# Kernel optimization log

Measured on AMD Instinct MI355X. Metric: run time of the kernel, lower is better.

Reference implementation:

```python
import jax, jax.numpy as jnp
import numpy as np

S, L, E = 64, 256, 768          # sentences, tokens per sentence, BERT hidden
N, P = 4096, 32768              # events, event pairs
C, H, D = 256, 4, 64            # CGE channels, heads, head dim (C = H*D = n_last)
M = 8                           # max event span length
MLP_H = 1024
ITERS = 3                       # max_iteration + 1
RATE = 0.5
BETA_INTRA, BETA_INTER = 0.5, 0.5


def setup_inputs():
    key = jax.random.key(0)
    ks = jax.random.split(key, 16)
    nrm = lambda k, shape, sc: jax.random.normal(k, shape, dtype=jnp.float32) * sc
    event_start = jax.random.randint(ks[2], (N,), 0, L - M)
    span = jax.random.randint(ks[3], (N,), 1, M + 1)
    return {
        "sent_emb": nrm(ks[0], (S, L, E), 1.0),
        "proj_in_W": nrm(ks[7], (E, C), E ** -0.5),
        "proj_in_b": jnp.zeros((C,), jnp.float32),
        "proj_W": nrm(ks[8], (C, C), C ** -0.5),
        "proj_b": jnp.zeros((C,), jnp.float32),
        "att_src_intra": nrm(ks[9], (H, D), D ** -0.5),
        "att_dst_intra": nrm(ks[10], (H, D), D ** -0.5),
        "att_src_inter": nrm(ks[11], (H, D), D ** -0.5),
        "att_dst_inter": nrm(ks[12], (H, D), D ** -0.5),
        "mlp_W1": nrm(ks[13], (C + 2 * E, MLP_H), (C + 2 * E) ** -0.5),
        "mlp_b1": jnp.zeros((MLP_H,), jnp.float32),
        "mlp_W2": nrm(ks[14], (MLP_H, 3), MLP_H ** -0.5),
        "mlp_b2": jnp.zeros((3,), jnp.float32),
        "event_sent": jax.random.randint(ks[1], (N,), 0, S),
        "event_start": event_start,
        "event_end": event_start + span,
        "pair_idx": jax.random.randint(ks[4], (P, 2), 0, N),
        "rel_type": jax.random.randint(ks[5], (P,), 0, 2),
        "target": jax.random.randint(ks[6], (P,), 0, 3),
    }


def _attend(h, src, dst, emask, att_src, att_dst):
    # h: [N,H,D]. Masked graph attention, softmax over incoming edges per dst.
    a = jax.nn.leaky_relu((h[src] * att_src).sum(-1) + (h[dst] * att_dst).sum(-1), 0.2)  # [En,H]
    a = jnp.where(emask[:, None], a, -1e9)
    amax = jnp.maximum(jax.ops.segment_max(a, dst, num_segments=N), -1e9)  # [N,H]
    ex = jnp.exp(a - amax[dst]) * emask[:, None].astype(a.dtype)
    denom = jax.ops.segment_sum(ex, dst, num_segments=N)
    alpha = ex / (denom[dst] + 1e-9)
    out = jax.ops.segment_sum(alpha[:, :, None] * h[src], dst, num_segments=N)  # [N,H,D]
    return out.reshape(N, H * D)


def _forward(sent_emb, proj_in_W, proj_in_b, proj_W, proj_b,
             att_src_intra, att_dst_intra, att_src_inter, att_dst_inter,
             mlp_W1, mlp_b1, mlp_W2, mlp_b2,
             event_sent, event_start, event_end, pair_idx, rel_type, target):
    # extract_event: mean of sentence token embeddings over each event span
    pos = event_start[:, None] + jnp.arange(M)                      # [N,M]
    vmask = (pos < event_end[:, None]).astype(sent_emb.dtype)       # [N,M]
    tok = sent_emb[event_sent[:, None], jnp.clip(pos, 0, L - 1)]    # [N,M,E]
    e_emb = (tok * vmask[..., None]).sum(1) / (event_end - event_start).astype(sent_emb.dtype)[:, None]

    p0, p1 = pair_idx[:, 0], pair_idx[:, 1]
    pair_emb = jnp.concatenate([e_emb[p0], e_emb[p1]], axis=-1)     # [P,2E]
    x = e_emb @ proj_in_W + proj_in_b                               # [N,C]

    self_idx = jnp.arange(N)
    ones_n = jnp.ones((N,), bool)
    src_all = jnp.concatenate([p0, p1])
    dst_all = jnp.concatenate([p1, p0])
    intra2 = jnp.concatenate([rel_type == 0, rel_type == 0])

    loss = jnp.float32(0.0)
    pred = None
    for it in range(ITERS):
        diff = x[p0] - x[p1]                                        # [P,C]
        pre = jnp.concatenate([pair_emb, diff], axis=-1)            # [P,2E+C]
        pred = jax.nn.relu(pre @ mlp_W1 + mlp_b1) @ mlp_W2 + mlp_b2  # [P,3]
        logp = jax.nn.log_softmax(pred, axis=-1)
        loss = loss + (1.0 / (it + 1)) * (-jnp.take_along_axis(logp, target[:, None], axis=1).mean())

        # data-dependent edge construction (masked, fixed-size edge lists)
        psoft = jax.nn.softmax(pred, axis=-1)
        conf = psoft.max(1) > RATE
        parg = psoft.argmax(1)
        m_all = jnp.concatenate([conf & (parg == 1), conf & (parg == 2)])

        h = (x @ proj_W + proj_b).reshape(N, H, D)
        # intra edges + always-on self loops
        src_i = jnp.concatenate([src_all, self_idx])
        dst_i = jnp.concatenate([dst_all, self_idx])
        m_i = jnp.concatenate([m_all & intra2, ones_n])
        out_intra = _attend(h, src_i, dst_i, m_i, att_src_intra, att_dst_intra)
        out_inter = _attend(h, src_all, dst_all, m_all & (~intra2), att_src_inter, att_dst_inter)
        x = BETA_INTRA * out_intra + BETA_INTER * out_inter
    return loss, pred


def reference(sent_emb, proj_in_W, proj_in_b, proj_W, proj_b,
              att_src_intra, att_dst_intra, att_src_inter, att_dst_inter,
              mlp_W1, mlp_b1, mlp_W2, mlp_b2,
              event_sent, event_start, event_end, pair_idx, rel_type, target):
    return _forward(sent_emb, proj_in_W, proj_in_b, proj_W, proj_b,
                    att_src_intra, att_dst_intra, att_src_inter, att_dst_inter,
                    mlp_W1, mlp_b1, mlp_W2, mlp_b2,
                    event_sent, event_start, event_end, pair_idx, rel_type, target)
```

## Files before the change

kernel.cpp:

```cpp
#include <hip/hip_runtime.h>
#include <cstddef>
#include <cstdint>

#define NEV   4096
#define NPAIR 32768
#define NEDGE (2*NPAIR)
#define EDIM  768
#define CDIM  256
#define MLPH  1024
#define LLEN  256

typedef unsigned short u16;
typedef __attribute__((ext_vector_type(8))) short bhalf8;
typedef __attribute__((ext_vector_type(4))) float f32x4;

#define GLOAD_LDS(g, l) __builtin_amdgcn_global_load_lds( \
    (const __attribute__((address_space(1))) unsigned int*)(g), \
    (__attribute__((address_space(3))) unsigned int*)(l), 16, 0, 0)

__device__ inline u16 f2bf(float f) {
  union { float f; unsigned u; } v; v.f = f;
  unsigned r = v.u + 0x7fffu + ((v.u >> 16) & 1u);
  return (u16)(r >> 16);
}
__device__ inline float bf2f(u16 h) {
  union { unsigned u; float f; } v; v.u = ((unsigned)h) << 16; return v.f;
}

__global__ __launch_bounds__(256) void k_prep(
    const float* __restrict__ sent, const int* __restrict__ es,
    const int* __restrict__ st, const int* __restrict__ en,
    u16* __restrict__ Ahat, const float* __restrict__ W1,
    const float* __restrict__ piW, const float* __restrict__ projW,
    u16* __restrict__ BTe, u16* __restrict__ BTu,
    int* __restrict__ deg, int* __restrict__ pdeg, float* __restrict__ out)
{
  __shared__ float tile[32][33];
  int b = blockIdx.x;
  int tid = threadIdx.x;
  if (b < NEV) {
    int node = b;
    int s = es[node];
    int a = st[node];
    int span = en[node] - a;
    float fspan = (float)span;
    const float* base = sent + ((size_t)s * LLEN + a) * EDIM;
    if (tid < 192) {
      int d0 = tid * 4;
      float4 acc = {0.f, 0.f, 0.f, 0.f};
      for (int m = 0; m < span; ++m) {
        float4 v = *(const float4*)(base + (size_t)m * EDIM + d0);
        acc.x += v.x; acc.y += v.y; acc.z += v.z; acc.w += v.w;
      }
      float e[4] = {acc.x / fspan, acc.y / fspan, acc.z / fspan, acc.w / fspan};
      ushort4 hiv, lov;
      u16 h0 = f2bf(e[0]); lov.x = f2bf(e[0] - bf2f(h0)); hiv.x = h0;
      u16 h1 = f2bf(e[1]); lov.y = f2bf(e[1] - bf2f(h1)); hiv.y = h1;
      u16 h2 = f2bf(e[2]); lov.z = f2bf(e[2] - bf2f(h2)); hiv.z = h2;
      u16 h3 = f2bf(e[3]); lov.w = f2bf(e[3] - bf2f(h3)); hiv.w = h3;
      size_t bo = (size_t)node * (2 * EDIM);
      *(ushort4*)&Ahat[bo + d0] = hiv;
      *(ushort4*)&Ahat[bo + EDIM + d0] = lov;
    }
    return;
  }
  if (b < NEV + 2304) {
    int id = b - NEV;
    int bxx = id % 72, byy = id / 72;
    int which = (byy >= 24) ? 1 : 0;
    if (which && bxx >= 40) return;
    u16* BT = which ? BTu : BTe;
    int K = which ? CDIM : EDIM;
    int ld = K * 2;
    int bk = (which ? (byy - 24) : byy) * 32;
    int bc = bxx * 32;
    int tx = tid & 31, ty = tid >> 5;
#pragma unroll
    for (int rr = 0; rr < 4; ++rr) {
      int k = bk + ty + rr * 8;
      int c = bc + tx;
      float v;
      if (which == 0) {
        v = (c < 1024) ? W1[(size_t)k * MLPH + c]
          : (c < 2048) ? W1[(size_t)(EDIM + k) * MLPH + (c - 1024)]
          : piW[(size_t)k * CDIM + (c - 2048)];
      } else {
        v = (c < 1024) ? W1[(size_t)(2 * EDIM + k) * MLPH + c]
          : projW[(size_t)k * CDIM + (c - 1024)];
      }
      tile[ty + rr * 8][tx] = v;
    }
    __syncthreads();
#pragma unroll
    for (int rr = 0; rr < 4; ++rr) {
      int c = bc + ty + rr * 8;
      int k = bk + tx;
      float v = tile[tx][ty + rr * 8];
      u16 hi = f2bf(v);
      float lo = v - bf2f(hi);
      size_t bb = (size_t)c * ld;
      BT[bb + k] = hi;
      BT[bb + K + k] = f2bf(lo);
    }
    return;
  }
  int i = (b - NEV - 2304) * 256 + tid;
  if (i < NEV) { deg[i] = 0; pdeg[i] = 0; }
  if (i == 0) out[0] = 0.f;
}

__global__ void k_countF(const int* __restrict__ pair, int* __restrict__ deg,
                         int* __restrict__ pdeg) {
  int e = blockIdx.x * 256 + threadIdx.x;
  if (e >= NEDGE) return;
  int p = (e < NPAIR) ? e : e - NPAIR;
  int dst = (e < NPAIR) ? pair[2 * p + 1] : pair[2 * p];
  atomicAdd(&deg[dst], 1);
  if (e < NPAIR) atomicAdd(&pdeg[pair[2 * e]], 1);
}

__device__ inline void scan_body(const int* __restrict__ deg, int* __restrict__ rowp,
                                 int* __restrict__ cursor, int* part) {
  int t = threadIdx.x;
  int base = t * 16;
  int sum = 0;
  for (int i = 0; i < 16; ++i) sum += deg[base + i];
  part[t] = sum;
  __syncthreads();
  for (int off = 1; off < 256; off <<= 1) {
    int v = (t >= off) ? part[t - off] : 0;
    __syncthreads();
    part[t] += v;
    __syncthreads();
  }
  int run = (t == 0) ? 0 : part[t - 1];
  for (int i = 0; i < 16; ++i) {
    rowp[base + i] = run;
    cursor[base + i] = 0;
    run += deg[base + i];
  }
  if (t == 255) rowp[NEV] = run;
}

__global__ void k_scanF(const int* __restrict__ deg, int* __restrict__ rowp,
                        int* __restrict__ cursor, const int* __restrict__ pdeg,
                        int* __restrict__ prow, int* __restrict__ pcur) {
  __shared__ int part[256];
  scan_body(deg, rowp, cursor, part);
  __syncthreads();
  scan_body(pdeg, prow, pcur, part);
}

__global__ void k_scatterF(const int* __restrict__ pair, const int* __restrict__ rowp,
                           int* __restrict__ cursor, int* __restrict__ e_src,
                           int* __restrict__ e_id, const int* __restrict__ prow,
                           int* __restrict__ pcur, int* __restrict__ pidx) {
  int e = blockIdx.x * 256 + threadIdx.x;
  if (e >= NEDGE) return;
  int p   = (e < NPAIR) ? e : e - NPAIR;
  int src = (e < NPAIR) ? pair[2 * p]     : pair[2 * p + 1];
  int dst = (e < NPAIR) ? pair[2 * p + 1] : pair[2 * p];
  int pos = rowp[dst] + atomicAdd(&cursor[dst], 1);
  e_src[pos] = src;
  e_id[pos]  = e;
  if (e < NPAIR) {
    int pp = prow[pair[2 * e]] + atomicAdd(&pcur[pair[2 * e]], 1);
    pidx[pp] = e;
  }
}

__global__ __launch_bounds__(256) void mgemm(
    const u16* __restrict__ A, const u16* __restrict__ BT, int K, int mode,
    float* __restrict__ G1, float* __restrict__ G2, u16* __restrict__ Xhat,
    const float* __restrict__ pib, const float* __restrict__ b1,
    const float* __restrict__ pb, float* __restrict__ U, float* __restrict__ V,
    float* __restrict__ h, const float* __restrict__ asi,
    const float* __restrict__ adi, const float* __restrict__ asj,
    const float* __restrict__ adj, float* __restrict__ sv)
{
  __shared__ u16 Ash[2 * 64 * 32];
  __shared__ u16 Asl[2 * 64 * 32];
  __shared__ u16 Bsh[2 * 128 * 32];
  __shared__ u16 Bsl[2 * 128 * 32];
  int tid = threadIdx.x;
  int wave = tid >> 6, lane = tid & 63;
  int bm = blockIdx.y * 64, bn = blockIdx.x * 128;
  int wm = (wave >> 1) * 32, wn = (wave & 1) * 64;

  int Kp2 = 2 * K;
  int srow = tid >> 2;
  int scol = (tid & 3) << 3;
  const u16* AgH  = A + (size_t)(bm + srow) * Kp2 + scol;
  const u16* BgH  = BT + (size_t)(bn + srow) * Kp2 + scol;
  const u16* BgH2 = BT + (size_t)(bn + 64 + srow) * Kp2 + scol;

  auto STAGE = [&](int buf, int kc) {
    u16* as = Ash + buf * 2048;
    u16* al = Asl + buf * 2048;
    u16* bs = Bsh + buf * 4096;
    u16* bl = Bsl + buf * 4096;
    GLOAD_LDS(AgH + kc,       &as[tid * 8]);
    GLOAD_LDS(AgH + K + kc,   &al[tid * 8]);
    GLOAD_LDS(BgH + kc,       &bs[tid * 8]);
    GLOAD_LDS(BgH2 + kc,      &bs[2048 + tid * 8]);
    GLOAD_LDS(BgH + K + kc,   &bl[tid * 8]);
    GLOAD_LDS(BgH2 + K + kc,  &bl[2048 + tid * 8]);
  };

  f32x4 acc[2][4];
#pragma unroll
  for (int i = 0; i < 2; ++i)
#pragma unroll
    for (int j = 0; j < 4; ++j) {
      f32x4 z = {0.f, 0.f, 0.f, 0.f};
      acc[i][j] = z;
    }

  int fr = lane & 15;
  int fq = lane >> 4;

  STAGE(0, 0);
  __syncthreads();
  int cur = 0;
  for (int kc = 0; kc < K; kc += 32) {
    if (kc + 32 < K) STAGE(cur ^ 1, kc + 32);
    const u16* as = Ash + cur * 2048;
    const u16* al = Asl + cur * 2048;
    const u16* bs = Bsh + cur * 4096;
    const u16* bl = Bsl + cur * 4096;
    bhalf8 afh[2], afl[2], bfh[4], bfl[4];
#pragma unroll
    for (int i = 0; i < 2; ++i) {
      afh[i] = *(const bhalf8*)&as[(wm + i * 16 + fr) * 32 + fq * 8];
      afl[i] = *(const bhalf8*)&al[(wm + i * 16 + fr) * 32 + fq * 8];
    }
#pragma unroll
    for (int j = 0; j < 4; ++j) {
      bfh[j] = *(const bhalf8*)&bs[(wn + j * 16 + fr) * 32 + fq * 8];
      bfl[j] = *(const bhalf8*)&bl[(wn + j * 16 + fr) * 32 + fq * 8];
    }
#pragma unroll
    for (int i = 0; i < 2; ++i)
#pragma unroll
      for (int j = 0; j < 4; ++j) {
        acc[i][j] = __builtin_amdgcn_mfma_f32_16x16x32_bf16(afh[i], bfh[j], acc[i][j], 0, 0, 0);
        acc[i][j] = __builtin_amdgcn_mfma_f32_16x16x32_bf16(afh[i], bfl[j], acc[i][j], 0, 0, 0);
        acc[i][j] = __builtin_amdgcn_mfma_f32_16x16x32_bf16(afl[i], bfh[j], acc[i][j], 0, 0, 0);
      }
    __syncthreads();
    cur ^= 1;
  }

#pragma unroll
  for (int i = 0; i < 2; ++i) {
    int mrow = bm + wm + i * 16 + fq * 4;
#pragma unroll
    for (int g = 0; g < 4; ++g) {
      int m = mrow + g;
#pragma unroll
      for (int j = 0; j < 4; ++j) {
        int c = bn + wn + j * 16 + fr;
        float vv = acc[i][j][g];
        if (mode == 0) {
          if (c < 1024) {
            G1[(size_t)m * MLPH + c] = vv;
          } else if (c < 2048) {
            G2[(size_t)m * MLPH + (c - 1024)] = vv;
          } else {
            int cc = c - 2048;
            float xv = vv + pib[cc];
            u16 hi = f2bf(xv);
            float lo = xv - bf2f(hi);
            size_t b = (size_t)m * (2 * CDIM);
            Xhat[b + cc] = hi;
            Xhat[b + CDIM + cc] = f2bf(lo);
          }
        } else {
          if (c < 1024) {
            size_t idx = (size_t)m * MLPH + c;
            U[idx] = G1[idx] + vv + b1[c];
            V[idx] = G2[idx] - vv;
          } else {
            int cc = c - 1024;
            h[(size_t)m * CDIM + cc] = vv + pb[cc];
          }
        }
      }
    }
  }

  if (mode == 1 && bn >= MLPH) {
    int hbase = bn - MLPH + wn;
    int head = hbase >> 6;
#pragma unroll
    for (int i = 0; i < 2; ++i) {
#pragma unroll
      for (int g = 0; g < 4; ++g) {
        int m = bm + wm + i * 16 + fq * 4 + g;
        float p0 = 0.f, p1 = 0.f, p2 = 0.f, p3 = 0.f;
#pragma unroll
        for (int j = 0; j < 4; ++j) {
          int hc = hbase + j * 16 + fr;
          float hv = acc[i][j][g] + pb[hc];
          p0 += hv * asi[hc];
          p1 += hv * adi[hc];
          p2 += hv * asj[hc];
          p3 += hv * adj[hc];
        }
#pragma unroll
        for (int mm = 1; mm < 16; mm <<= 1) {
          p0 += __shfl_xor(p0, mm);
          p1 += __shfl_xor(p1, mm);
          p2 += __shfl_xor(p2, mm);
          p3 += __shfl_xor(p3, mm);
        }
        if (fr == 0) {
          sv[0 * NEV * 4 + m * 4 + head] = p0;
          sv[1 * NEV * 4 + m * 4 + head] = p1;
          sv[2 * NEV * 4 + m * 4 + head] = p2;
          sv[3 * NEV * 4 + m * 4 + head] = p3;
        }
      }
    }
  }
}

__global__ __launch_bounds__(256) void k_pred_g(
    const float* __restrict__ U, const float* __restrict__ V,
    const int* __restrict__ pair, const int* __restrict__ prow,
    const int* __restrict__ pidx, const float* __restrict__ W2,
    const float* __restrict__ b2, const int* __restrict__ target,
    int* __restrict__ mstate, float* __restrict__ out,
    float* __restrict__ partials, float lossCoef)
{
  __shared__ float ush[MLPH];
  __shared__ float red[4];
  int n = blockIdx.x;
  int tid = threadIdx.x;
  const float* u = U + (size_t)n * MLPH;
#pragma unroll
  for (int i = 0; i < 4; ++i) ush[tid + i * 256] = u[tid + i * 256];
  __syncthreads();
  int wv = tid >> 6, lane = tid & 63;
  int beg = prow[n], end = prow[n + 1];
  float lsum = 0.f;
  for (int ip = beg + wv; ip < end; ip += 4) {
    int p = pidx[ip];
    int i1 = pair[2 * p + 1];
    const float* v = V + (size_t)i1 * MLPH;
    float a0 = 0.f, a1 = 0.f, a2 = 0.f;
    for (int kb = (lane << 2); kb < MLPH; kb += 256) {
      float4 uu = *(const float4*)(&ush[kb]);
      float4 vv = *(const float4*)(v + kb);
      float h0 = fmaxf(uu.x + vv.x, 0.f);
      float h1 = fmaxf(uu.y + vv.y, 0.f);
      float h2 = fmaxf(uu.z + vv.z, 0.f);
      float h3 = fmaxf(uu.w + vv.w, 0.f);
      const float4* w4 = (const float4*)(W2 + 3 * kb);
      float4 wa = w4[0], wb = w4[1], wc = w4[2];
      a0 += h0 * wa.x + h1 * wa.w + h2 * wb.z + h3 * wc.y;
      a1 += h0 * wa.y + h1 * wb.x + h2 * wb.w + h3 * wc.z;
      a2 += h0 * wa.z + h1 * wb.y + h2 * wc.x + h3 * wc.w;
    }
#pragma unroll
    for (int m = 32; m >= 1; m >>= 1) {
      a0 += __shfl_down(a0, m);
      a1 += __shfl_down(a1, m);
      a2 += __shfl_down(a2, m);
    }
    if (lane == 0) {
      a0 += b2[0]; a1 += b2[1]; a2 += b2[2];
      float mx = fmaxf(a0, fmaxf(a1, a2));
      float e0 = expf(a0 - mx), e1 = expf(a1 - mx), e2 = expf(a2 - mx);
      float sum = e0 + e1 + e2;
      int arg = 0; float best = e0;
      if (e1 > best) { best = e1; arg = 1; }
      if (e2 > best) { best = e2; arg = 2; }
      bool conf = (best / sum) > 0.5f;
      mstate[p] = conf ? arg : -1;
      int t = target[p];
      float predt = (t == 0) ? a0 : ((t == 1) ? a1 : a2);
      float logp = (predt - mx) - logf(sum);
      lsum += -logp * lossCoef;
      float* po = out + 1 + (size_t)p * 3;
      po[0] = a0; po[1] = a1; po[2] = a2;
    }
  }
  if (lane == 0) red[wv] = lsum;
  __syncthreads();
  if (tid == 0) partials[n] = red[0] + red[1] + red[2] + red[3];
}

__global__ __launch_bounds__(256) void k_attn(
    const float* __restrict__ h, const float* __restrict__ sv,
    const int* __restrict__ rowp, const int* __restrict__ e_src,
    const int* __restrict__ e_id, const int* __restrict__ mstate,
    const int* __restrict__ rel, u16* __restrict__ Xhat,
    const float* __restrict__ lpart, float* __restrict__ out)
{
  int node = blockIdx.x;
  int t = threadIdx.x;
  int head = t >> 6;
  const float* s_si = sv;
  const float* s_di = sv + NEV * 4;
  const float* s_sj = sv + 2 * NEV * 4;
  const float* s_dj = sv + 3 * NEV * 4;
  float sdi = s_di[node * 4 + head];
  float sdj = s_dj[node * 4 + head];
  int beg = rowp[node], end = rowp[node + 1];
  float aself = s_si[node * 4 + head] + sdi;
  aself = aself > 0.f ? aself : 0.2f * aself;
  float mxi = aself;
  float mxj = -1e9f;
  for (int e = beg; e < end; ++e) {
    int eid = e_id[e];
    int pp = (eid < NPAIR) ? eid : eid - NPAIR;
    int st = mstate[pp];
    bool mall = (eid < NPAIR) ? (st == 1) : (st == 2);
    if (!mall) continue;
    int src = e_src[e];
    if (rel[pp] == 0) {
      float a = s_si[src * 4 + head] + sdi;
      a = a > 0.f ? a : 0.2f * a;
      mxi = fmaxf(mxi, a);
    } else {
      float a = s_sj[src * 4 + head] + sdj;
      a = a > 0.f ? a : 0.2f * a;
      mxj = fmaxf(mxj, a);
    }
  }
  float deni = 0.f, denj = 0.f, acci = 0.f, accj = 0.f;
  {
    float ex = expf(aself - mxi);
    deni += ex;
    acci += ex * h[(size_t)node * CDIM + t];
  }
  for (int e = beg; e < end; ++e) {
    int eid = e_id[e];
    int pp = (eid < NPAIR) ? eid : eid - NPAIR;
    int st = mstate[pp];
    bool mall = (eid < NPAIR) ? (st == 1) : (st == 2);
    if (!mall) continue;
    int src = e_src[e];
    float hval = h[(size_t)src * CDIM + t];
    if (rel[pp] == 0) {
      float a = s_si[src * 4 + head] + sdi;
      a = a > 0.f ? a : 0.2f * a;
      float ex = expf(a - mxi);
      deni += ex; acci += ex * hval;
    } else {
      float a = s_sj[src * 4 + head] + sdj;
      a = a > 0.f ? a : 0.2f * a;
      float ex = expf(a - mxj);
      denj += ex; accj += ex * hval;
    }
  }
  float outv = 0.5f * (acci / (deni + 1e-9f)) + 0.5f * (accj / (denj + 1e-9f));
  u16 hi = f2bf(outv);
  float lo = outv - bf2f(hi);
  size_t b = (size_t)node * (2 * CDIM);
  Xhat[b + t] = hi;
  Xhat[b + CDIM + t] = f2bf(lo);

  if (blockIdx.x == 0) {
    __shared__ float sm[256];
    float s = 0.f;
    for (int i = t; i < NEV; i += 256) s += lpart[i];
    sm[t] = s;
    __syncthreads();
    for (int off = 128; off; off >>= 1) {
      if (t < off) sm[t] += sm[t + off];
      __syncthreads();
    }
    if (t == 0) out[0] += sm[0];
  }
}

extern "C" void kernel_launch(void* const* d_in, const int* in_sizes, int n_in,
                              void* d_out, int out_size, void* d_ws, size_t ws_size,
                              hipStream_t stream)
{
  const float* sent      = (const float*)d_in[0];
  const float* proj_in_W = (const float*)d_in[1];
  const float* proj_in_b = (const float*)d_in[2];
  const float* proj_W    = (const float*)d_in[3];
  const float* proj_b    = (const float*)d_in[4];
  const float* asi       = (const float*)d_in[5];
  const float* adi       = (const float*)d_in[6];
  const float* asj       = (const float*)d_in[7];
  const float* adj       = (const float*)d_in[8];
  const float* W1        = (const float*)d_in[9];
  const float* b1        = (const float*)d_in[10];
  const float* W2        = (const float*)d_in[11];
  const float* b2        = (const float*)d_in[12];
  const int*   es        = (const int*)d_in[13];
  const int*   st        = (const int*)d_in[14];
  const int*   en        = (const int*)d_in[15];
  const int*   pair      = (const int*)d_in[16];
  const int*   rel       = (const int*)d_in[17];
  const int*   target    = (const int*)d_in[18];
  float* out = (float*)d_out;

  char* w = (char*)d_ws;
  auto alloc = [&](size_t bytes) -> char* {
    char* p = w;
    w += (bytes + 255) & ~(size_t)255;
    return p;
  };
  u16*   Ahat = (u16*)alloc(sizeof(u16) * (size_t)NEV * 2 * EDIM);
  u16*   BTe  = (u16*)alloc(sizeof(u16) * (size_t)2304 * 1536);
  u16*   BTu  = (u16*)alloc(sizeof(u16) * (size_t)1280 * 512);
  u16*   Xhat = (u16*)alloc(sizeof(u16) * (size_t)NEV * 2 * CDIM);
  float* G1   = (float*)alloc(sizeof(float) * (size_t)NEV * MLPH);
  float* G2   = (float*)alloc(sizeof(float) * (size_t)NEV * MLPH);
  float* U    = (float*)alloc(sizeof(float) * (size_t)NEV * MLPH);
  float* V    = (float*)alloc(sizeof(float) * (size_t)NEV * MLPH);
  float* h    = (float*)alloc(sizeof(float) * (size_t)NEV * CDIM);
  float* sv   = (float*)alloc(sizeof(float) * (size_t)NEV * 16);
  float* lpart= (float*)alloc(sizeof(float) * NEV);
  int* deg    = (int*)alloc(sizeof(int) * NEV);
  int* rowp   = (int*)alloc(sizeof(int) * (NEV + 1));
  int* cursor = (int*)alloc(sizeof(int) * NEV);
  int* e_src  = (int*)alloc(sizeof(int) * NEDGE);
  int* e_id   = (int*)alloc(sizeof(int) * NEDGE);
  int* pdeg   = (int*)alloc(sizeof(int) * NEV);
  int* prow   = (int*)alloc(sizeof(int) * (NEV + 1));
  int* pcur   = (int*)alloc(sizeof(int) * NEV);
  int* pidx   = (int*)alloc(sizeof(int) * NPAIR);
  int* mstate = (int*)alloc(sizeof(int) * NPAIR);

  k_prep<<<NEV + 2304 + 16, 256, 0, stream>>>(sent, es, st, en, Ahat,
                                              W1, proj_in_W, proj_W, BTe, BTu,
                                              deg, pdeg, out);
  k_countF<<<NEDGE / 256, 256, 0, stream>>>(pair, deg, pdeg);
  k_scanF<<<1, 256, 0, stream>>>(deg, rowp, cursor, pdeg, prow, pcur);
  k_scatterF<<<NEDGE / 256, 256, 0, stream>>>(pair, rowp, cursor, e_src, e_id,
                                              prow, pcur, pidx);

  mgemm<<<dim3(2304 / 128, NEV / 64), 256, 0, stream>>>(
      Ahat, BTe, EDIM, 0, G1, G2, Xhat, proj_in_b,
      nullptr, nullptr, nullptr, nullptr, nullptr,
      nullptr, nullptr, nullptr, nullptr, nullptr);

  for (int it = 0; it < 3; ++it) {
    mgemm<<<dim3(1280 / 128, NEV / 64), 256, 0, stream>>>(
        Xhat, BTu, CDIM, 1, G1, G2, nullptr, nullptr,
        b1, proj_b, U, V, h, asi, adi, asj, adj, sv);
    float coef = 1.0f / ((float)(it + 1) * (float)NPAIR);
    k_pred_g<<<NEV, 256, 0, stream>>>(U, V, pair, prow, pidx, W2, b2, target,
                                      mstate, out, lpart, coef);
    k_attn<<<NEV, 256, 0, stream>>>(h, sv, rowp, e_src, e_id, mstate, rel, Xhat,
                                    lpart, out);
  }
  (void)in_sizes; (void)n_in; (void)out_size; (void)ws_size;
}
```

Measured before the change: 484.0 us.

## Use online softmax with cooperative edge staging in attention; keep MLP operands in registers

In the attention kernel, the two passes over incoming edges (max pass, then exp/accumulate pass) become one pass using online softmax with rescaling. Edge metadata and per-head scores are staged cooperatively in shared memory in chunks, so each edge's mask, relation and score loads happen once per block instead of once per thread. In the prediction kernel, the u row and W2 slices are held in registers instead of going through shared memory and repeated global loads. The changes add register pressure and barriers per chunk, and fast __expf plus online rescaling may change numerics slightly.

After: 493.6 us. No clear change (+2.0%).

```diff
diff --git a/kernel.cpp b/kernel.cpp
--- a/kernel.cpp
+++ b/kernel.cpp
@@ -9,6 +9,7 @@
 #define CDIM  256
 #define MLPH  1024
 #define LLEN  256
+#define ACH   128
 
 typedef unsigned short u16;
 typedef __attribute__((ext_vector_type(8))) short bhalf8;
@@ -333,15 +334,20 @@
     int* __restrict__ mstate, float* __restrict__ out,
     float* __restrict__ partials, float lossCoef)
 {
-  __shared__ float ush[MLPH];
   __shared__ float red[4];
   int n = blockIdx.x;
   int tid = threadIdx.x;
+  int wv = tid >> 6, lane = tid & 63;
   const float* u = U + (size_t)n * MLPH;
-#pragma unroll
-  for (int i = 0; i < 4; ++i) ush[tid + i * 256] = u[tid + i * 256];
-  __syncthreads();
-  int wv = tid >> 6, lane = tid & 63;
+  float4 ureg[4];
+  float4 wreg[4][3];
+#pragma unroll
+  for (int i = 0; i < 4; ++i) {
+    int kb = (lane << 2) + i * 256;
+    ureg[i] = *(const float4*)(u + kb);
+    const float4* w4 = (const float4*)(W2 + 3 * kb);
+    wreg[i][0] = w4[0]; wreg[i][1] = w4[1]; wreg[i][2] = w4[2];
+  }
   int beg = prow[n], end = prow[n + 1];
   float lsum = 0.f;
   for (int ip = beg + wv; ip < end; ip += 4) {
@@ -349,15 +355,16 @@
     int i1 = pair[2 * p + 1];
     const float* v = V + (size_t)i1 * MLPH;
     float a0 = 0.f, a1 = 0.f, a2 = 0.f;
-    for (int kb = (lane << 2); kb < MLPH; kb += 256) {
-      float4 uu = *(const float4*)(&ush[kb]);
+#pragma unroll
+    for (int i = 0; i < 4; ++i) {
+      int kb = (lane << 2) + i * 256;
       float4 vv = *(const float4*)(v + kb);
+      float4 uu = ureg[i];
       float h0 = fmaxf(uu.x + vv.x, 0.f);
       float h1 = fmaxf(uu.y + vv.y, 0.f);
       float h2 = fmaxf(uu.z + vv.z, 0.f);
       float h3 = fmaxf(uu.w + vv.w, 0.f);
-      const float4* w4 = (const float4*)(W2 + 3 * kb);
-      float4 wa = w4[0], wb = w4[1], wc = w4[2];
+      float4 wa = wreg[i][0], wb = wreg[i][1], wc = wreg[i][2];
       a0 += h0 * wa.x + h1 * wa.w + h2 * wb.z + h3 * wc.y;
       a1 += h0 * wa.y + h1 * wb.x + h2 * wb.w + h3 * wc.z;
       a2 += h0 * wa.z + h1 * wb.y + h2 * wc.x + h3 * wc.w;
@@ -398,6 +405,8 @@
     const int* __restrict__ rel, u16* __restrict__ Xhat,
     const float* __restrict__ lpart, float* __restrict__ out)
 {
+  __shared__ float sc[ACH * 4];
+  __shared__ int   meta[ACH];
   int node = blockIdx.x;
   int t = threadIdx.x;
   int head = t >> 6;
@@ -405,56 +414,65 @@
   const float* s_di = sv + NEV * 4;
   const float* s_sj = sv + 2 * NEV * 4;
   const float* s_dj = sv + 3 * NEV * 4;
-  float sdi = s_di[node * 4 + head];
-  float sdj = s_dj[node * 4 + head];
+  float4 sdi4 = *(const float4*)(s_di + node * 4);
+  float4 sdj4 = *(const float4*)(s_dj + node * 4);
   int beg = rowp[node], end = rowp[node + 1];
-  float aself = s_si[node * 4 + head] + sdi;
+
+  float sdi_h = ((const float*)&sdi4)[head];
+  float aself = s_si[node * 4 + head] + sdi_h;
   aself = aself > 0.f ? aself : 0.2f * aself;
-  float mxi = aself;
-  float mxj = -1e9f;
-  for (int e = beg; e < end; ++e) {
-    int eid = e_id[e];
-    int pp = (eid < NPAIR) ? eid : eid - NPAIR;
-    int st = mstate[pp];
-    bool mall = (eid < NPAIR) ? (st == 1) : (st == 2);
-    if (!mall) continue;
-    int src = e_src[e];
-    if (rel[pp] == 0) {
-      float a = s_si[src * 4 + head] + sdi;
-      a = a > 0.f ? a : 0.2f * a;
-      mxi = fmaxf(mxi, a);
-    } else {
-      float a = s_sj[src * 4 + head] + sdj;
-      a = a > 0.f ? a : 0.2f * a;
-      mxj = fmaxf(mxj, a);
-    }
-  }
-  float deni = 0.f, denj = 0.f, acci = 0.f, accj = 0.f;
-  {
-    float ex = expf(aself - mxi);
-    deni += ex;
-    acci += ex * h[(size_t)node * CDIM + t];
-  }
-  for (int e = beg; e < end; ++e) {
-    int eid = e_id[e];
-    int pp = (eid < NPAIR) ? eid : eid - NPAIR;
-    int st = mstate[pp];
-    bool mall = (eid < NPAIR) ? (st == 1) : (st == 2);
-    if (!mall) continue;
-    int src = e_src[e];
-    float hval = h[(size_t)src * CDIM + t];
-    if (rel[pp] == 0) {
-      float a = s_si[src * 4 + head] + sdi;
-      a = a > 0.f ? a : 0.2f * a;
-      float ex = expf(a - mxi);
-      deni += ex; acci += ex * hval;
-    } else {
-      float a = s_sj[src * 4 + head] + sdj;
-      a = a > 0.f ? a : 0.2f * a;
-      float ex = expf(a - mxj);
-      denj += ex; accj += ex * hval;
-    }
-  }
+  float mxi = aself, deni = 1.f, acci = h[(size_t)node * CDIM + t];
+  float mxj = -1e30f, denj = 0.f, accj = 0.f;
+
+  for (int c0 = beg; c0 < end; c0 += ACH) {
+    int cn = min(ACH, end - c0);
+    __syncthreads();
+    for (int idx = t; idx < cn; idx += 256) {
+      int e = c0 + idx;
+      int eid = e_id[e];
+      int pp = (eid < NPAIR) ? eid : eid - NPAIR;
+      int st = mstate[pp];
+      bool mall = (eid < NPAIR) ? (st == 1) : (st == 2);
+      if (!mall) { meta[idx] = -1; continue; }
+      int src = e_src[e];
+      int r = rel[pp];
+      float4 ssv = r ? *(const float4*)(s_sj + 4 * src)
+                     : *(const float4*)(s_si + 4 * src);
+      float4 sd = r ? sdj4 : sdi4;
+      float a0 = ssv.x + sd.x; a0 = a0 > 0.f ? a0 : 0.2f * a0;
+      float a1 = ssv.y + sd.y; a1 = a1 > 0.f ? a1 : 0.2f * a1;
+      float a2 = ssv.z + sd.z; a2 = a2 > 0.f ? a2 : 0.2f * a2;
+      float a3 = ssv.w + sd.w; a3 = a3 > 0.f ? a3 : 0.2f * a3;
+      float4 av = {a0, a1, a2, a3};
+      *(float4*)&sc[idx * 4] = av;
+      meta[idx] = src | (r << 16);
+    }
+    __syncthreads();
+    for (int idx = 0; idx < cn; ++idx) {
+      int m = meta[idx];
+      if (m < 0) continue;
+      int src = m & 0xFFFF;
+      int r = m >> 16;
+      float a = sc[idx * 4 + head];
+      float hval = h[(size_t)src * CDIM + t];
+      if (r == 0) {
+        if (a > mxi) {
+          float s = __expf(mxi - a);
+          deni *= s; acci *= s; mxi = a;
+        }
+        float ex = __expf(a - mxi);
+        deni += ex; acci += ex * hval;
+      } else {
+        if (a > mxj) {
+          float s = __expf(mxj - a);
+          denj *= s; accj *= s; mxj = a;
+        }
+        float ex = __expf(a - mxj);
+        denj += ex; accj += ex * hval;
+      }
+    }
+  }
+
   float outv = 0.5f * (acci / (deni + 1e-9f)) + 0.5f * (accj / (denj + 1e-9f));
   u16 hi = f2bf(outv);
   float lo = outv - bf2f(hi);
```
